# Kernel tuning notes

Hardware: AMD Instinct MI355X
Metric: run time of the kernel (lower is better)

The kernel has to match this reference:

```python
import jax, jax.numpy as jnp
import numpy as np

B, N, F, D, H, T = 32, 1024, 32, 64, 64, 4


def setup_inputs() -> dict:
    key = jax.random.key(0)
    ks = jax.random.split(key, 12)
    def w(k, shape):
        return 0.01 * jax.random.normal(k, shape, dtype=jnp.float32)
    z = lambda *s: jnp.zeros(s, jnp.float32)
    return {
        "xv": jax.random.normal(ks[0], (B, N, F), dtype=jnp.float32),
        "option": jax.random.uniform(ks[1], (B, 1), dtype=jnp.float32),
        "adj": jax.random.normal(ks[2], (N, N), dtype=jnp.float32),
        "mu1": w(ks[3], (F, D)),
        "W2": w(ks[4], (D, D)), "b2": z(D),
        "W3": w(ks[5], (D, D)), "b3": z(D),
        "W4": w(ks[6], (D, 1)), "b4": z(D),
        "Wq1": w(ks[7], (D, D)), "bq1": z(D),
        "Wq2": w(ks[8], (D, 1)), "bq2": z(D),
        "Wreg": w(ks[9], (H, 2 * D)), "breg": z(H),
        "Wq": w(ks[10], (1, H)), "bq": z(1),
    }


def reference(xv, option, adj, mu1, W2, b2, W3, b3, W4, b4,
              Wq1, bq1, Wq2, bq2, Wreg, breg, Wq, bq):
    # binary adjacency for message passing, raw weights for the mu_4 branch
    A = (adj > 0).astype(xv.dtype)                       # [N,N]
    mu_1 = jnp.maximum(xv @ mu1, 0.0)                    # [B,N,D]
    # mu_4: Linear(1,D) over every edge weight, clamp, sum over neighbors
    # (identical value every round t>=1, so computed once)
    mu4 = jnp.maximum(adj[..., None] * W4[:, 0] + b4, 0.0).sum(axis=1)[None]  # [1,N,D]
    mu3 = mu4 @ W3.T + b3                                # [1,N,D]
    mu = mu_1                                            # t = 0
    for _ in range(1, T):                                # t = 1..T-1
        mu_pool = jnp.einsum('nm,bmd->bnd', A, mu)       # neighbor aggregation
        mu2 = mu_pool @ W2.T + b2
        mu = jnp.maximum(mu_1 + mu2 + mu3, 0.0)
    mu_mean = jnp.maximum(mu.mean(axis=1, keepdims=True) @ Wq1.T + bq1, 0.0)  # [B,1,D]
    mu_aug = jnp.concatenate([mu, mu_mean], axis=1)      # [B,N+1,D]
    q2 = option.reshape(B, 1, 1) @ Wq2.T + bq2           # [B,1,D]
    q2 = jnp.broadcast_to(q2, (B, N + 1, D))
    q_ = jnp.concatenate([mu_aug, q2], axis=-1)          # [B,N+1,2D]
    qreg = jnp.maximum(q_ @ Wreg.T + breg, 0.0)          # [B,N+1,H]
    return qreg @ Wq.T + bq                              # [B,N+1,1]
```

## Files before the change

### kernel.cpp

```cpp
#include <hip/hip_runtime.h>
#include <hip/hip_bf16.h>

#define Bc 32
#define Nc 1024
#define Fc 32
#define Dc 64
#define Hc 64

typedef __bf16 bf16;
typedef __bf16 bf16x4 __attribute__((ext_vector_type(4)));
typedef __bf16 bf16x8 __attribute__((ext_vector_type(8)));
typedef float  f32x4  __attribute__((ext_vector_type(4)));

#define MS 72
#define LDS_RND_NONF 18432
#define LDS_RND_FIN  37376


__global__ void k_init(const float* __restrict__ adj, const float* __restrict__ W4,
                       const float* __restrict__ b4, const float* __restrict__ W3,
                       const float* __restrict__ b3, const float* __restrict__ b2,
                       const float* __restrict__ W2, const float* __restrict__ option,
                       const float* __restrict__ Wq2, const float* __restrict__ bq2,
                       const float* __restrict__ Wreg, const float* __restrict__ breg,
                       const float* __restrict__ xv, const float* __restrict__ mu1w,
                       bf16* __restrict__ Afrag, float* __restrict__ C3,
                       bf16* __restrict__ W2bf, float* __restrict__ c2base,
                       float* __restrict__ musum,
                       float* __restrict__ mu_1, bf16* __restrict__ Xfrag0) {
    const int id = blockIdx.x, t = threadIdx.x;
    __shared__ char smem[39424];
    if (id < 1024) {
        const int n = id;
        float* red   = (float*)smem;
        float* mu4_s = red + 256;
        const float* arow = adj + (size_t)n * Nc;
        {
            const int m0 = t * 4;
            const float4 a = *(const float4*)&arow[m0];
            bf16x4 o;
            o[0] = (bf16)((a.x > 0.f) ? 1.f : 0.f);
            o[1] = (bf16)((a.y > 0.f) ? 1.f : 0.f);
            o[2] = (bf16)((a.z > 0.f) ? 1.f : 0.f);
            o[3] = (bf16)((a.w > 0.f) ? 1.f : 0.f);
            const int g = n >> 4, lm = n & 15;
            const int k0 = m0 >> 5, q = (m0 & 31) >> 3, j = m0 & 7;
            *(bf16x4*)&Afrag[(size_t)((g * 32 + k0) * 64 + lm + 16 * q) * 8 + j] = o;
        }
        const int e = t & 63, g = t >> 6;
        const float w4e = W4[e], b4e = b4[e];
        float acc = 0.f;
        const float4* arow4 = (const float4*)(arow + g * 256);
#pragma unroll 8
        for (int j = 0; j < 64; ++j) {
            const float4 av = arow4[j];
            acc += fmaxf(fmaf(av.x, w4e, b4e), 0.f);
            acc += fmaxf(fmaf(av.y, w4e, b4e), 0.f);
            acc += fmaxf(fmaf(av.z, w4e, b4e), 0.f);
            acc += fmaxf(fmaf(av.w, w4e, b4e), 0.f);
        }
        red[t] = acc;
        __syncthreads();
        if (g == 0) mu4_s[e] = red[e] + red[64 + e] + red[128 + e] + red[192 + e];
        __syncthreads();
        if (t < 64) {
            const int d = t;
            float a = b3[d] + b2[d];
#pragma unroll
            for (int ee = 0; ee < 64; ++ee) a = fmaf(mu4_s[ee], W3[d * 64 + ee], a);
            C3[n * 64 + d] = a;
        }
    } else if (id == 1024) {
        for (int j = t * 16; j < t * 16 + 16; ++j) W2bf[j] = (bf16)W2[j];
        for (int i = t; i < 2048; i += 256) musum[i] = 0.f;
        for (int i = t; i < 2048; i += 256) {
            const int b = i >> 6, h = i & 63;
            const float opt = option[b];
            float a = breg[h];
#pragma unroll
            for (int j = 0; j < 64; ++j)
                a = fmaf(fmaf(opt, Wq2[j], bq2[j]), Wreg[h * 128 + 64 + j], a);
            c2base[i] = a;
        }
    } else {
        const int idx = id - 1025, nb = idx & 15, b = idx >> 4;
        const int n0 = nb * 64;
        const int l = t & 63, wv = t >> 6, lm = l & 15, q = l >> 4;
        bf16* W2s = (bf16*)smem;
        bf16* xhi = (bf16*)(smem + 9216);
        bf16* xlo = (bf16*)(smem + 14336);
        bf16* whi = (bf16*)(smem + 19456);
        bf16* wlo = (bf16*)(smem + 24576);
        bf16* muS = (bf16*)(smem + 29696);
        {
            const int row = t >> 2, f0 = (t & 3) * 8;
            const float* src = &xv[((size_t)b * Nc + n0 + row) * Fc + f0];
            const float4 v0 = *(const float4*)src;
            const float4 v1 = *(const float4*)(src + 4);
            bf16x8 hi, lo;
            float vv[8] = {v0.x, v0.y, v0.z, v0.w, v1.x, v1.y, v1.z, v1.w};
#pragma unroll
            for (int j = 0; j < 8; ++j) { hi[j] = (bf16)vv[j]; lo[j] = (bf16)(vv[j] - (float)hi[j]); }
            *(bf16x8*)&xhi[row * 40 + f0] = hi;
            *(bf16x8*)&xlo[row * 40 + f0] = lo;
        }
        {
            const int d = t >> 2, f0 = (t & 3) * 8;
#pragma unroll
            for (int j = 0; j < 8; ++j) {
                const float v = mu1w[(f0 + j) * Dc + d];
                const bf16 hi = (bf16)v;
                whi[d * 40 + f0 + j] = hi;
                wlo[d * 40 + f0 + j] = (bf16)(v - (float)hi);
            }
        }
        {
            const int row = t >> 2, c0 = (t & 3) * 16;
            const float4 v0 = *(const float4*)&W2[row * 64 + c0];
            const float4 v1 = *(const float4*)&W2[row * 64 + c0 + 4];
            const float4 v2 = *(const float4*)&W2[row * 64 + c0 + 8];
            const float4 v3 = *(const float4*)&W2[row * 64 + c0 + 12];
            bf16x8 p0, p1;
            p0[0]=(bf16)v0.x; p0[1]=(bf16)v0.y; p0[2]=(bf16)v0.z; p0[3]=(bf16)v0.w;
            p0[4]=(bf16)v1.x; p0[5]=(bf16)v1.y; p0[6]=(bf16)v1.z; p0[7]=(bf16)v1.w;
            p1[0]=(bf16)v2.x; p1[1]=(bf16)v2.y; p1[2]=(bf16)v2.z; p1[3]=(bf16)v2.w;
            p1[4]=(bf16)v3.x; p1[5]=(bf16)v3.y; p1[6]=(bf16)v3.z; p1[7]=(bf16)v3.w;
            *(bf16x8*)&W2s[row * MS + c0] = p0;
            *(bf16x8*)&W2s[row * MS + c0 + 8] = p1;
        }
        __syncthreads();
        f32x4 acc[4];
#pragma unroll
        for (int ct = 0; ct < 4; ++ct)
#pragma unroll
            for (int r = 0; r < 4; ++r) acc[ct][r] = 0.f;
        {
            const bf16x8 aHi = *(const bf16x8*)&xhi[(wv * 16 + lm) * 40 + q * 8];
            const bf16x8 aLo = *(const bf16x8*)&xlo[(wv * 16 + lm) * 40 + q * 8];
#pragma unroll
            for (int ct = 0; ct < 4; ++ct) {
                const bf16x8 bHi = *(const bf16x8*)&whi[(ct * 16 + lm) * 40 + q * 8];
                const bf16x8 bLo = *(const bf16x8*)&wlo[(ct * 16 + lm) * 40 + q * 8];
                acc[ct] = __builtin_amdgcn_mfma_f32_16x16x32_bf16(aHi, bHi, acc[ct], 0, 0, 0);
                acc[ct] = __builtin_amdgcn_mfma_f32_16x16x32_bf16(aLo, bHi, acc[ct], 0, 0, 0);
                acc[ct] = __builtin_amdgcn_mfma_f32_16x16x32_bf16(aHi, bLo, acc[ct], 0, 0, 0);
            }
        }
#pragma unroll
        for (int ct = 0; ct < 4; ++ct) {
            const int col = ct * 16 + lm;
#pragma unroll
            for (int r = 0; r < 4; ++r) {
                const int row = wv * 16 + q * 4 + r;
                const float v = fmaxf(acc[ct][r], 0.f);
                mu_1[((size_t)b * Nc + n0 + row) * Dc + col] = v;
                muS[row * MS + col] = (bf16)v;
            }
        }
        __syncthreads();
        f32x4 xacc[4];
#pragma unroll
        for (int ct = 0; ct < 4; ++ct)
#pragma unroll
            for (int r = 0; r < 4; ++r) xacc[ct][r] = 0.f;
#pragma unroll
        for (int s = 0; s < 2; ++s) {
            bf16x8 a = *(const bf16x8*)&muS[(wv * 16 + lm) * MS + s * 32 + q * 8];
#pragma unroll
            for (int ct = 0; ct < 4; ++ct) {
                bf16x8 bv = *(const bf16x8*)&W2s[(ct * 16 + lm) * MS + s * 32 + q * 8];
                xacc[ct] = __builtin_amdgcn_mfma_f32_16x16x32_bf16(a, bv, xacc[ct], 0, 0, 0);
            }
        }
        const int k0 = nb * 2 + (wv >> 1);
        const int q_c = (wv & 1) * 2 + (q >> 1);
        const int j0 = (q & 1) * 4;
#pragma unroll
        for (int ct = 0; ct < 4; ++ct) {
            bf16x4 p;
#pragma unroll
            for (int r = 0; r < 4; ++r) p[r] = (bf16)xacc[ct][r];
            *(bf16x4*)&Xfrag0[(size_t)b * 65536
                              + (size_t)((ct * 32 + k0) * 64 + lm + 16 * q_c) * 8 + j0] = p;
        }
    }
}

template <bool FINAL>
__global__ __launch_bounds__(256, 2)
void k_round(const bf16* __restrict__ Afrag, const bf16* __restrict__ Xfr_in,
             const float* __restrict__ mu_1, const float* __restrict__ C3,
             const bf16* __restrict__ W2bf, bf16* __restrict__ Xfr_out,
             const float* __restrict__ Wreg, const float* __restrict__ c2base,
             const float* __restrict__ Wq, const float* __restrict__ bq,
             float* __restrict__ musum, float* __restrict__ out) {
    const int id = blockIdx.x, t = threadIdx.x;
    const int b  = ((id & 7) << 2) | ((id >> 3) & 3);
    const int nb = id >> 5;
    const int n0 = nb * 64;
    const int l = t & 63, wv = t >> 6, lm = l & 15, q = l >> 4;
    const int rh = wv & 1, ch = wv >> 1;
    extern __shared__ char smem[];
    bf16* muHi = (bf16*)smem;
    bf16* muLo = (bf16*)(smem + 9216);
    bf16* WHi  = (bf16*)(smem + (FINAL ? 18432 : 9216));
    bf16* WLo  = (bf16*)(smem + 27648);
    float* rpart = (float*)(smem + 36864);

    if (!FINAL) {
#pragma unroll
        for (int i = 0; i < 2; ++i) {
            int g = i * 256 + t, row = g >> 3, c = g & 7;
            *(bf16x8*)&WHi[row * MS + c * 8] = *(const bf16x8*)&W2bf[row * 64 + c * 8];
        }
    } else {
#pragma unroll
        for (int i = 0; i < 4; ++i) {
            int g = i * 1024 + t * 4, h = g >> 6, d = g & 63;
            const float4 w4 = *(const float4*)&Wreg[h * 128 + d];
            bf16x4 ohi, olo;
            ohi[0] = (bf16)w4.x; olo[0] = (bf16)(w4.x - (float)ohi[0]);
            ohi[1] = (bf16)w4.y; olo[1] = (bf16)(w4.y - (float)ohi[1]);
            ohi[2] = (bf16)w4.z; olo[2] = (bf16)(w4.z - (float)ohi[2]);
            ohi[3] = (bf16)w4.w; olo[3] = (bf16)(w4.w - (float)ohi[3]);
            *(bf16x4*)&WHi[h * MS + d] = ohi;
            *(bf16x4*)&WLo[h * MS + d] = olo;
        }
    }

    f32x4 acc[2][2];
#pragma unroll
    for (int rt = 0; rt < 2; ++rt)
#pragma unroll
        for (int ct = 0; ct < 2; ++ct)
#pragma unroll
            for (int r = 0; r < 4; ++r) acc[rt][ct][r] = 0.f;

    const int gA = nb * 4 + rh * 2;
    const bf16* pa0 = Afrag + (size_t)(gA + 0) * 32 * 512 + l * 8;
    const bf16* pa1 = Afrag + (size_t)(gA + 1) * 32 * 512 + l * 8;
    const bf16* px0 = Xfr_in + (size_t)b * 65536 + (size_t)(ch * 2 + 0) * 32 * 512 + l * 8;
    const bf16* px1 = Xfr_in + (size_t)b * 65536 + (size_t)(ch * 2 + 1) * 32 * 512 + l * 8;
#pragma unroll 4
    for (int k0 = 0; k0 < 32; ++k0) {
        const int o = k0 * 512;
        bf16x8 a0 = *(const bf16x8*)&pa0[o];
        bf16x8 a1 = *(const bf16x8*)&pa1[o];
        bf16x8 x0 = *(const bf16x8*)&px0[o];
        bf16x8 x1 = *(const bf16x8*)&px1[o];
        acc[0][0] = __builtin_amdgcn_mfma_f32_16x16x32_bf16(a0, x0, acc[0][0], 0, 0, 0);
        acc[0][1] = __builtin_amdgcn_mfma_f32_16x16x32_bf16(a0, x1, acc[0][1], 0, 0, 0);
        acc[1][0] = __builtin_amdgcn_mfma_f32_16x16x32_bf16(a1, x0, acc[1][0], 0, 0, 0);
        acc[1][1] = __builtin_amdgcn_mfma_f32_16x16x32_bf16(a1, x1, acc[1][1], 0, 0, 0);
    }

    float vals[2][2][4];
#pragma unroll
    for (int rt = 0; rt < 2; ++rt)
#pragma unroll
        for (int ct = 0; ct < 2; ++ct) {
            const int col = ch * 32 + ct * 16 + lm;
#pragma unroll
            for (int r = 0; r < 4; ++r) {
                const int n = n0 + rh * 32 + rt * 16 + q * 4 + r;
                float v = mu_1[((size_t)b * Nc + n) * Dc + col] + acc[rt][ct][r]
                        + C3[n * 64 + col];
                vals[rt][ct][r] = fmaxf(v, 0.f);
            }
        }

#pragma unroll
    for (int rt = 0; rt < 2; ++rt)
#pragma unroll
        for (int ct = 0; ct < 2; ++ct) {
            const int col = ch * 32 + ct * 16 + lm;
#pragma unroll
            for (int r = 0; r < 4; ++r) {
                const int row = rh * 32 + rt * 16 + q * 4 + r;
                const float v = vals[rt][ct][r];
                const bf16 hi = (bf16)v;
                muHi[row * MS + col] = hi;
                if (FINAL) muLo[row * MS + col] = (bf16)(v - (float)hi);
            }
        }
    if (FINAL) {
#pragma unroll
        for (int ct = 0; ct < 2; ++ct) {
            float s = 0.f;
#pragma unroll
            for (int rt = 0; rt < 2; ++rt)
#pragma unroll
                for (int r = 0; r < 4; ++r) s += vals[rt][ct][r];
            s += __shfl_xor(s, 16);
            s += __shfl_xor(s, 32);
            if (q == 0) atomicAdd(&musum[b * 64 + ch * 32 + ct * 16 + lm], s);
        }
    }
    __syncthreads();

    f32x4 xacc[2][2];
#pragma unroll
    for (int rt = 0; rt < 2; ++rt)
#pragma unroll
        for (int ct = 0; ct < 2; ++ct)
#pragma unroll
            for (int r = 0; r < 4; ++r) xacc[rt][ct][r] = 0.f;

    if (!FINAL) {
#pragma unroll
        for (int s = 0; s < 2; ++s) {
            bf16x8 aM[2], bW[2];
#pragma unroll
            for (int rt = 0; rt < 2; ++rt)
                aM[rt] = *(const bf16x8*)&muHi[(rh * 32 + rt * 16 + lm) * MS + s * 32 + q * 8];
#pragma unroll
            for (int ct = 0; ct < 2; ++ct)
                bW[ct] = *(const bf16x8*)&WHi[(ch * 32 + ct * 16 + lm) * MS + s * 32 + q * 8];
#pragma unroll
            for (int rt = 0; rt < 2; ++rt)
#pragma unroll
                for (int ct = 0; ct < 2; ++ct)
                    xacc[rt][ct] = __builtin_amdgcn_mfma_f32_16x16x32_bf16(aM[rt], bW[ct],
                                                                           xacc[rt][ct], 0, 0, 0);
        }
        const int k0 = nb * 2 + rh;
        const int q_c0 = (q >> 1), j0 = (q & 1) * 4;
#pragma unroll
        for (int rt = 0; rt < 2; ++rt)
#pragma unroll
            for (int ct = 0; ct < 2; ++ct) {
                bf16x4 p;
#pragma unroll
                for (int r = 0; r < 4; ++r) p[r] = (bf16)xacc[rt][ct][r];
                *(bf16x4*)&Xfr_out[(size_t)b * 65536
                    + (size_t)(((ch * 2 + ct) * 32 + k0) * 64 + lm + 16 * (rt * 2 + q_c0)) * 8
                    + j0] = p;
            }
    } else {
#pragma unroll
        for (int s = 0; s < 2; ++s) {
            bf16x8 aH[2], aL[2], bH[2], bL[2];
#pragma unroll
            for (int rt = 0; rt < 2; ++rt) {
                const int ao = (rh * 32 + rt * 16 + lm) * MS + s * 32 + q * 8;
                aH[rt] = *(const bf16x8*)&muHi[ao];
                aL[rt] = *(const bf16x8*)&muLo[ao];
            }
#pragma unroll
            for (int ct = 0; ct < 2; ++ct) {
                const int bo = (ch * 32 + ct * 16 + lm) * MS + s * 32 + q * 8;
                bH[ct] = *(const bf16x8*)&WHi[bo];
                bL[ct] = *(const bf16x8*)&WLo[bo];
            }
#pragma unroll
            for (int rt = 0; rt < 2; ++rt)
#pragma unroll
                for (int ct = 0; ct < 2; ++ct) {
                    xacc[rt][ct] = __builtin_amdgcn_mfma_f32_16x16x32_bf16(aH[rt], bH[ct],
                                                                           xacc[rt][ct], 0, 0, 0);
                    xacc[rt][ct] = __builtin_amdgcn_mfma_f32_16x16x32_bf16(aL[rt], bH[ct],
                                                                           xacc[rt][ct], 0, 0, 0);
                    xacc[rt][ct] = __builtin_amdgcn_mfma_f32_16x16x32_bf16(aH[rt], bL[ct],
                                                                           xacc[rt][ct], 0, 0, 0);
                }
        }
        const float bq0 = bq[0];
        float rowsum[2][4] = {{0.f, 0.f, 0.f, 0.f}, {0.f, 0.f, 0.f, 0.f}};
#pragma unroll
        for (int ct = 0; ct < 2; ++ct) {
            const int h = ch * 32 + ct * 16 + lm;
            const float c2 = c2base[b * 64 + h];
            const float wqh = Wq[h];
#pragma unroll
            for (int rt = 0; rt < 2; ++rt)
#pragma unroll
                for (int r = 0; r < 4; ++r)
                    rowsum[rt][r] += fmaxf(xacc[rt][ct][r] + c2, 0.f) * wqh;
        }
#pragma unroll
        for (int rt = 0; rt < 2; ++rt)
#pragma unroll
            for (int r = 0; r < 4; ++r) {
                float v = rowsum[rt][r];
                v += __shfl_xor(v, 1);
                v += __shfl_xor(v, 2);
                v += __shfl_xor(v, 4);
                v += __shfl_xor(v, 8);
                if (lm == 0) rpart[ch * 64 + rh * 32 + rt * 16 + q * 4 + r] = v;
            }
        __syncthreads();
        if (t < 64)
            out[(size_t)b * (Nc + 1) + n0 + t] = rpart[t] + rpart[64 + t] + bq0;
    }
}

__global__ void k_tail(const float* __restrict__ musum, const float* __restrict__ Wq1,
                       const float* __restrict__ bq1, const float* __restrict__ Wreg,
                       const float* __restrict__ c2base, const float* __restrict__ Wq,
                       const float* __restrict__ bq, float* __restrict__ out) {
    const int b = blockIdx.x, l = threadIdx.x;
    __shared__ float mean_s[64];
    __shared__ float mp[64];
    mean_s[l] = musum[b * 64 + l] * (1.f / Nc);
    __syncthreads();
    float a = bq1[l];
#pragma unroll
    for (int e = 0; e < 64; ++e) a = fmaf(mean_s[e], Wq1[l * 64 + e], a);
    mp[l] = fmaxf(a, 0.f);
    __syncthreads();
    float h = c2base[b * 64 + l];
#pragma unroll
    for (int d = 0; d < 64; ++d) h = fmaf(mp[d], Wreg[l * 128 + d], h);
    float v = fmaxf(h, 0.f) * Wq[l];
#pragma unroll
    for (int off = 32; off; off >>= 1) v += __shfl_down(v, off);
    if (l == 0) out[(size_t)b * (Nc + 1) + Nc] = v + bq[0];
}

extern "C" void kernel_launch(void* const* d_in, const int* in_sizes, int n_in,
                              void* d_out, int out_size, void* d_ws, size_t ws_size,
                              hipStream_t stream) {
    const float* xv     = (const float*)d_in[0];
    const float* option = (const float*)d_in[1];
    const float* adj    = (const float*)d_in[2];
    const float* mu1w   = (const float*)d_in[3];
    const float* W2     = (const float*)d_in[4];
    const float* b2     = (const float*)d_in[5];
    const float* W3     = (const float*)d_in[6];
    const float* b3     = (const float*)d_in[7];
    const float* W4     = (const float*)d_in[8];
    const float* b4     = (const float*)d_in[9];
    const float* Wq1    = (const float*)d_in[10];
    const float* bq1    = (const float*)d_in[11];
    const float* Wq2    = (const float*)d_in[12];
    const float* bq2    = (const float*)d_in[13];
    const float* Wreg   = (const float*)d_in[14];
    const float* breg   = (const float*)d_in[15];
    const float* Wq     = (const float*)d_in[16];
    const float* bq     = (const float*)d_in[17];
    float* out = (float*)d_out;

    float* ws = (float*)d_ws;
    const size_t MU = (size_t)Bc * Nc * Dc;
    float* mu_1     = ws;
    float* C3       = ws + MU;
    float* c2base   = C3 + 65536;
    float* musum    = c2base + 2048;
    bf16*  Afrag    = (bf16*)(musum + 2048);
    bf16*  W2bf     = Afrag + (size_t)Nc * Nc;
    bf16*  Xf0      = W2bf + 4096;
    bf16*  Xf1      = Xf0 + MU;

    k_init<<<1537, 256, 0, stream>>>(adj, W4, b4, W3, b3, b2, W2, option, Wq2, bq2,
                                     Wreg, breg, xv, mu1w,
                                     Afrag, C3, W2bf, c2base, musum, mu_1, Xf0);
    k_round<false><<<512, 256, LDS_RND_NONF, stream>>>(
        Afrag, Xf0, mu_1, C3, W2bf, Xf1,
        nullptr, nullptr, nullptr, nullptr, nullptr, nullptr);
    k_round<false><<<512, 256, LDS_RND_NONF, stream>>>(
        Afrag, Xf1, mu_1, C3, W2bf, Xf0,
        nullptr, nullptr, nullptr, nullptr, nullptr, nullptr);
    k_round<true><<<512, 256, LDS_RND_FIN, stream>>>(
        Afrag, Xf0, mu_1, C3, nullptr, nullptr,
        Wreg, c2base, Wq, bq, musum, out);
    k_tail<<<Bc, 64, 0, stream>>>(musum, Wq1, bq1, Wreg, c2base, Wq, bq, out);
}
```

Measured before the change: 154.8 us.

## Fuse all stages into one persistent kernel with software grid barriers

Merges the init, three message-passing rounds and tail kernels into a single persistent kernel of 512 blocks. The blocks synchronise through an atomic counter barrier that is reset with a memset before launch. The init work is redistributed so each block handles two adjacency rows plus one xv tile, and W3 is staged transposed in LDS. The aim is to remove the launch gaps and tail effects between the five kernels. In exchange it depends on all 512 blocks being co-resident, and the barrier has a timeout guard that could silently break correctness.

Result: slower. 343.1 us (+121.7%).

```diff
diff --git a/kernel.cpp b/kernel.cpp
--- a/kernel.cpp
+++ b/kernel.cpp
@@ -6,6 +6,7 @@
 #define Fc 32
 #define Dc 64
 #define Hc 64
+#define NBLK 512
 
 typedef __bf16 bf16;
 typedef __bf16 bf16x4 __attribute__((ext_vector_type(4)));
@@ -13,207 +14,46 @@
 typedef float  f32x4  __attribute__((ext_vector_type(4)));
 
 #define MS 72
-#define LDS_RND_NONF 18432
-#define LDS_RND_FIN  37376
-
-
-__global__ void k_init(const float* __restrict__ adj, const float* __restrict__ W4,
-                       const float* __restrict__ b4, const float* __restrict__ W3,
-                       const float* __restrict__ b3, const float* __restrict__ b2,
-                       const float* __restrict__ W2, const float* __restrict__ option,
-                       const float* __restrict__ Wq2, const float* __restrict__ bq2,
-                       const float* __restrict__ Wreg, const float* __restrict__ breg,
-                       const float* __restrict__ xv, const float* __restrict__ mu1w,
-                       bf16* __restrict__ Afrag, float* __restrict__ C3,
-                       bf16* __restrict__ W2bf, float* __restrict__ c2base,
-                       float* __restrict__ musum,
-                       float* __restrict__ mu_1, bf16* __restrict__ Xfrag0) {
-    const int id = blockIdx.x, t = threadIdx.x;
-    __shared__ char smem[39424];
-    if (id < 1024) {
-        const int n = id;
-        float* red   = (float*)smem;
-        float* mu4_s = red + 256;
-        const float* arow = adj + (size_t)n * Nc;
-        {
-            const int m0 = t * 4;
-            const float4 a = *(const float4*)&arow[m0];
-            bf16x4 o;
-            o[0] = (bf16)((a.x > 0.f) ? 1.f : 0.f);
-            o[1] = (bf16)((a.y > 0.f) ? 1.f : 0.f);
-            o[2] = (bf16)((a.z > 0.f) ? 1.f : 0.f);
-            o[3] = (bf16)((a.w > 0.f) ? 1.f : 0.f);
-            const int g = n >> 4, lm = n & 15;
-            const int k0 = m0 >> 5, q = (m0 & 31) >> 3, j = m0 & 7;
-            *(bf16x4*)&Afrag[(size_t)((g * 32 + k0) * 64 + lm + 16 * q) * 8 + j] = o;
-        }
-        const int e = t & 63, g = t >> 6;
-        const float w4e = W4[e], b4e = b4[e];
-        float acc = 0.f;
-        const float4* arow4 = (const float4*)(arow + g * 256);
-#pragma unroll 8
-        for (int j = 0; j < 64; ++j) {
-            const float4 av = arow4[j];
-            acc += fmaxf(fmaf(av.x, w4e, b4e), 0.f);
-            acc += fmaxf(fmaf(av.y, w4e, b4e), 0.f);
-            acc += fmaxf(fmaf(av.z, w4e, b4e), 0.f);
-            acc += fmaxf(fmaf(av.w, w4e, b4e), 0.f);
-        }
-        red[t] = acc;
-        __syncthreads();
-        if (g == 0) mu4_s[e] = red[e] + red[64 + e] + red[128 + e] + red[192 + e];
-        __syncthreads();
-        if (t < 64) {
-            const int d = t;
-            float a = b3[d] + b2[d];
-#pragma unroll
-            for (int ee = 0; ee < 64; ++ee) a = fmaf(mu4_s[ee], W3[d * 64 + ee], a);
-            C3[n * 64 + d] = a;
-        }
-    } else if (id == 1024) {
-        for (int j = t * 16; j < t * 16 + 16; ++j) W2bf[j] = (bf16)W2[j];
-        for (int i = t; i < 2048; i += 256) musum[i] = 0.f;
-        for (int i = t; i < 2048; i += 256) {
-            const int b = i >> 6, h = i & 63;
-            const float opt = option[b];
-            float a = breg[h];
-#pragma unroll
-            for (int j = 0; j < 64; ++j)
-                a = fmaf(fmaf(opt, Wq2[j], bq2[j]), Wreg[h * 128 + 64 + j], a);
-            c2base[i] = a;
-        }
-    } else {
-        const int idx = id - 1025, nb = idx & 15, b = idx >> 4;
-        const int n0 = nb * 64;
-        const int l = t & 63, wv = t >> 6, lm = l & 15, q = l >> 4;
-        bf16* W2s = (bf16*)smem;
-        bf16* xhi = (bf16*)(smem + 9216);
-        bf16* xlo = (bf16*)(smem + 14336);
-        bf16* whi = (bf16*)(smem + 19456);
-        bf16* wlo = (bf16*)(smem + 24576);
-        bf16* muS = (bf16*)(smem + 29696);
-        {
-            const int row = t >> 2, f0 = (t & 3) * 8;
-            const float* src = &xv[((size_t)b * Nc + n0 + row) * Fc + f0];
-            const float4 v0 = *(const float4*)src;
-            const float4 v1 = *(const float4*)(src + 4);
-            bf16x8 hi, lo;
-            float vv[8] = {v0.x, v0.y, v0.z, v0.w, v1.x, v1.y, v1.z, v1.w};
-#pragma unroll
-            for (int j = 0; j < 8; ++j) { hi[j] = (bf16)vv[j]; lo[j] = (bf16)(vv[j] - (float)hi[j]); }
-            *(bf16x8*)&xhi[row * 40 + f0] = hi;
-            *(bf16x8*)&xlo[row * 40 + f0] = lo;
-        }
-        {
-            const int d = t >> 2, f0 = (t & 3) * 8;
-#pragma unroll
-            for (int j = 0; j < 8; ++j) {
-                const float v = mu1w[(f0 + j) * Dc + d];
-                const bf16 hi = (bf16)v;
-                whi[d * 40 + f0 + j] = hi;
-                wlo[d * 40 + f0 + j] = (bf16)(v - (float)hi);
-            }
-        }
-        {
-            const int row = t >> 2, c0 = (t & 3) * 16;
-            const float4 v0 = *(const float4*)&W2[row * 64 + c0];
-            const float4 v1 = *(const float4*)&W2[row * 64 + c0 + 4];
-            const float4 v2 = *(const float4*)&W2[row * 64 + c0 + 8];
-            const float4 v3 = *(const float4*)&W2[row * 64 + c0 + 12];
-            bf16x8 p0, p1;
-            p0[0]=(bf16)v0.x; p0[1]=(bf16)v0.y; p0[2]=(bf16)v0.z; p0[3]=(bf16)v0.w;
-            p0[4]=(bf16)v1.x; p0[5]=(bf16)v1.y; p0[6]=(bf16)v1.z; p0[7]=(bf16)v1.w;
-            p1[0]=(bf16)v2.x; p1[1]=(bf16)v2.y; p1[2]=(bf16)v2.z; p1[3]=(bf16)v2.w;
-            p1[4]=(bf16)v3.x; p1[5]=(bf16)v3.y; p1[6]=(bf16)v3.z; p1[7]=(bf16)v3.w;
-            *(bf16x8*)&W2s[row * MS + c0] = p0;
-            *(bf16x8*)&W2s[row * MS + c0 + 8] = p1;
-        }
-        __syncthreads();
-        f32x4 acc[4];
-#pragma unroll
-        for (int ct = 0; ct < 4; ++ct)
-#pragma unroll
-            for (int r = 0; r < 4; ++r) acc[ct][r] = 0.f;
-        {
-            const bf16x8 aHi = *(const bf16x8*)&xhi[(wv * 16 + lm) * 40 + q * 8];
-            const bf16x8 aLo = *(const bf16x8*)&xlo[(wv * 16 + lm) * 40 + q * 8];
-#pragma unroll
-            for (int ct = 0; ct < 4; ++ct) {
-                const bf16x8 bHi = *(const bf16x8*)&whi[(ct * 16 + lm) * 40 + q * 8];
-                const bf16x8 bLo = *(const bf16x8*)&wlo[(ct * 16 + lm) * 40 + q * 8];
-                acc[ct] = __builtin_amdgcn_mfma_f32_16x16x32_bf16(aHi, bHi, acc[ct], 0, 0, 0);
-                acc[ct] = __builtin_amdgcn_mfma_f32_16x16x32_bf16(aLo, bHi, acc[ct], 0, 0, 0);
-                acc[ct] = __builtin_amdgcn_mfma_f32_16x16x32_bf16(aHi, bLo, acc[ct], 0, 0, 0);
-            }
-        }
-#pragma unroll
-        for (int ct = 0; ct < 4; ++ct) {
-            const int col = ct * 16 + lm;
-#pragma unroll
-            for (int r = 0; r < 4; ++r) {
-                const int row = wv * 16 + q * 4 + r;
-                const float v = fmaxf(acc[ct][r], 0.f);
-                mu_1[((size_t)b * Nc + n0 + row) * Dc + col] = v;
-                muS[row * MS + col] = (bf16)v;
-            }
-        }
-        __syncthreads();
-        f32x4 xacc[4];
-#pragma unroll
-        for (int ct = 0; ct < 4; ++ct)
-#pragma unroll
-            for (int r = 0; r < 4; ++r) xacc[ct][r] = 0.f;
-#pragma unroll
-        for (int s = 0; s < 2; ++s) {
-            bf16x8 a = *(const bf16x8*)&muS[(wv * 16 + lm) * MS + s * 32 + q * 8];
-#pragma unroll
-            for (int ct = 0; ct < 4; ++ct) {
-                bf16x8 bv = *(const bf16x8*)&W2s[(ct * 16 + lm) * MS + s * 32 + q * 8];
-                xacc[ct] = __builtin_amdgcn_mfma_f32_16x16x32_bf16(a, bv, xacc[ct], 0, 0, 0);
-            }
-        }
-        const int k0 = nb * 2 + (wv >> 1);
-        const int q_c = (wv & 1) * 2 + (q >> 1);
-        const int j0 = (q & 1) * 4;
-#pragma unroll
-        for (int ct = 0; ct < 4; ++ct) {
-            bf16x4 p;
-#pragma unroll
-            for (int r = 0; r < 4; ++r) p[r] = (bf16)xacc[ct][r];
-            *(bf16x4*)&Xfrag0[(size_t)b * 65536
-                              + (size_t)((ct * 32 + k0) * 64 + lm + 16 * q_c) * 8 + j0] = p;
-        }
-    }
+#define SMEM_BYTES 39424
+
+__device__ __forceinline__ void grid_sync(unsigned* bar, unsigned phase) {
+    __syncthreads();
+    if (threadIdx.x == 0) {
+        __threadfence();
+        atomicAdd(bar, 1u);
+        const unsigned tgt = (unsigned)NBLK * phase;
+        int guard = 0;
+        while (atomicAdd(bar, 0u) < tgt) {
+            __builtin_amdgcn_s_sleep(2);
+            if (++guard > (1 << 22)) break;
+        }
+        __threadfence();
+    }
+    __syncthreads();
 }
 
 template <bool FINAL>
-__global__ __launch_bounds__(256, 2)
-void k_round(const bf16* __restrict__ Afrag, const bf16* __restrict__ Xfr_in,
-             const float* __restrict__ mu_1, const float* __restrict__ C3,
-             const bf16* __restrict__ W2bf, bf16* __restrict__ Xfr_out,
-             const float* __restrict__ Wreg, const float* __restrict__ c2base,
-             const float* __restrict__ Wq, const float* __restrict__ bq,
-             float* __restrict__ musum, float* __restrict__ out) {
-    const int id = blockIdx.x, t = threadIdx.x;
+__device__ __forceinline__ void round_body(
+    char* smem, int id,
+    const bf16* __restrict__ Afrag, const bf16* __restrict__ Xfr_in,
+    const float* __restrict__ mu_1, const float* __restrict__ C3,
+    bf16* __restrict__ Xfr_out,
+    const float* __restrict__ Wreg, const float* __restrict__ c2base,
+    const float* __restrict__ Wq, const float* __restrict__ bq,
+    float* __restrict__ musum, float* __restrict__ out) {
+    const int t = threadIdx.x;
     const int b  = ((id & 7) << 2) | ((id >> 3) & 3);
     const int nb = id >> 5;
     const int n0 = nb * 64;
     const int l = t & 63, wv = t >> 6, lm = l & 15, q = l >> 4;
     const int rh = wv & 1, ch = wv >> 1;
-    extern __shared__ char smem[];
-    bf16* muHi = (bf16*)smem;
-    bf16* muLo = (bf16*)(smem + 9216);
-    bf16* WHi  = (bf16*)(smem + (FINAL ? 18432 : 9216));
+    bf16* WHi  = (bf16*)smem;
+    bf16* muHi = (bf16*)(smem + 9216);
+    bf16* muLo = (bf16*)(smem + 18432);
     bf16* WLo  = (bf16*)(smem + 27648);
     float* rpart = (float*)(smem + 36864);
 
-    if (!FINAL) {
-#pragma unroll
-        for (int i = 0; i < 2; ++i) {
-            int g = i * 256 + t, row = g >> 3, c = g & 7;
-            *(bf16x8*)&WHi[row * MS + c * 8] = *(const bf16x8*)&W2bf[row * 64 + c * 8];
-        }
-    } else {
+    if (FINAL) {
 #pragma unroll
         for (int i = 0; i < 4; ++i) {
             int g = i * 1024 + t * 4, h = g >> 6, d = g & 63;
@@ -394,27 +234,219 @@
     }
 }
 
-__global__ void k_tail(const float* __restrict__ musum, const float* __restrict__ Wq1,
-                       const float* __restrict__ bq1, const float* __restrict__ Wreg,
-                       const float* __restrict__ c2base, const float* __restrict__ Wq,
-                       const float* __restrict__ bq, float* __restrict__ out) {
-    const int b = blockIdx.x, l = threadIdx.x;
-    __shared__ float mean_s[64];
-    __shared__ float mp[64];
-    mean_s[l] = musum[b * 64 + l] * (1.f / Nc);
-    __syncthreads();
-    float a = bq1[l];
-#pragma unroll
-    for (int e = 0; e < 64; ++e) a = fmaf(mean_s[e], Wq1[l * 64 + e], a);
-    mp[l] = fmaxf(a, 0.f);
-    __syncthreads();
-    float h = c2base[b * 64 + l];
-#pragma unroll
-    for (int d = 0; d < 64; ++d) h = fmaf(mp[d], Wreg[l * 128 + d], h);
-    float v = fmaxf(h, 0.f) * Wq[l];
-#pragma unroll
-    for (int off = 32; off; off >>= 1) v += __shfl_down(v, off);
-    if (l == 0) out[(size_t)b * (Nc + 1) + Nc] = v + bq[0];
+__global__ __launch_bounds__(256, 2) void k_fused(
+    const float* __restrict__ adj, const float* __restrict__ W4,
+    const float* __restrict__ b4, const float* __restrict__ W3,
+    const float* __restrict__ b3, const float* __restrict__ b2,
+    const float* __restrict__ W2, const float* __restrict__ option,
+    const float* __restrict__ Wq2, const float* __restrict__ bq2,
+    const float* __restrict__ Wreg, const float* __restrict__ breg,
+    const float* __restrict__ xv, const float* __restrict__ mu1w,
+    const float* __restrict__ Wq1, const float* __restrict__ bq1,
+    const float* __restrict__ Wq, const float* __restrict__ bq,
+    bf16* __restrict__ Afrag, float* __restrict__ C3,
+    float* __restrict__ c2base, float* __restrict__ musum,
+    float* __restrict__ mu_1, bf16* __restrict__ Xf0, bf16* __restrict__ Xf1,
+    float* __restrict__ out, unsigned* __restrict__ bar) {
+    const int id = blockIdx.x, t = threadIdx.x;
+    extern __shared__ char smem[];
+
+    if (id < 8) {
+        musum[id * 256 + t] = 0.f;
+    } else if (id < 16) {
+        const int i = (id - 8) * 256 + t, b = i >> 6, h = i & 63;
+        const float opt = option[b];
+        float a = breg[h];
+#pragma unroll
+        for (int j = 0; j < 64; ++j)
+            a = fmaf(fmaf(opt, Wq2[j], bq2[j]), Wreg[h * 128 + 64 + j], a);
+        c2base[i] = a;
+    }
+    {
+        float* W3sT = (float*)smem;
+        float* red  = (float*)(smem + 16640);
+        float* mu4s = (float*)(smem + 17664);
+        for (int i = t; i < 4096; i += 256) {
+            const int r = i >> 6, c = i & 63;
+            W3sT[c * 65 + r] = W3[i];
+        }
+        for (int rr = 0; rr < 2; ++rr) {
+            const int n = id * 2 + rr;
+            const float* arow = adj + (size_t)n * Nc;
+            {
+                const int m0 = t * 4;
+                const float4 a = *(const float4*)&arow[m0];
+                bf16x4 o;
+                o[0] = (bf16)((a.x > 0.f) ? 1.f : 0.f);
+                o[1] = (bf16)((a.y > 0.f) ? 1.f : 0.f);
+                o[2] = (bf16)((a.z > 0.f) ? 1.f : 0.f);
+                o[3] = (bf16)((a.w > 0.f) ? 1.f : 0.f);
+                const int g = n >> 4, lm = n & 15;
+                const int k0 = m0 >> 5, qq = (m0 & 31) >> 3, j = m0 & 7;
+                *(bf16x4*)&Afrag[(size_t)((g * 32 + k0) * 64 + lm + 16 * qq) * 8 + j] = o;
+            }
+            const int e = t & 63, g = t >> 6;
+            const float w4e = W4[e], b4e = b4[e];
+            float acc = 0.f;
+            const float4* arow4 = (const float4*)(arow + g * 256);
+#pragma unroll 8
+            for (int j = 0; j < 64; ++j) {
+                const float4 av = arow4[j];
+                acc += fmaxf(fmaf(av.x, w4e, b4e), 0.f);
+                acc += fmaxf(fmaf(av.y, w4e, b4e), 0.f);
+                acc += fmaxf(fmaf(av.z, w4e, b4e), 0.f);
+                acc += fmaxf(fmaf(av.w, w4e, b4e), 0.f);
+            }
+            red[t] = acc;
+            __syncthreads();
+            if (g == 0) mu4s[e] = red[e] + red[64 + e] + red[128 + e] + red[192 + e];
+            __syncthreads();
+            if (t < 64) {
+                float a = b3[t] + b2[t];
+#pragma unroll
+                for (int ee = 0; ee < 64; ++ee) a = fmaf(mu4s[ee], W3sT[ee * 65 + t], a);
+                C3[n * 64 + t] = a;
+            }
+            __syncthreads();
+        }
+    }
+    {
+        const int nb = id & 15, b = id >> 4;
+        const int n0 = nb * 64;
+        const int l = t & 63, wv = t >> 6, lm = l & 15, q = l >> 4;
+        bf16* W2s = (bf16*)smem;
+        bf16* xhi = (bf16*)(smem + 9216);
+        bf16* xlo = (bf16*)(smem + 14336);
+        bf16* whi = (bf16*)(smem + 19456);
+        bf16* wlo = (bf16*)(smem + 24576);
+        bf16* muS = (bf16*)(smem + 29696);
+        {
+            const int row = t >> 2, f0 = (t & 3) * 8;
+            const float* src = &xv[((size_t)b * Nc + n0 + row) * Fc + f0];
+            const float4 v0 = *(const float4*)src;
+            const float4 v1 = *(const float4*)(src + 4);
+            bf16x8 hi, lo;
+            float vv[8] = {v0.x, v0.y, v0.z, v0.w, v1.x, v1.y, v1.z, v1.w};
+#pragma unroll
+            for (int j = 0; j < 8; ++j) { hi[j] = (bf16)vv[j]; lo[j] = (bf16)(vv[j] - (float)hi[j]); }
+            *(bf16x8*)&xhi[row * 40 + f0] = hi;
+            *(bf16x8*)&xlo[row * 40 + f0] = lo;
+        }
+        {
+            const int d = t >> 2, f0 = (t & 3) * 8;
+#pragma unroll
+            for (int j = 0; j < 8; ++j) {
+                const float v = mu1w[(f0 + j) * Dc + d];
+                const bf16 hi = (bf16)v;
+                whi[d * 40 + f0 + j] = hi;
+                wlo[d * 40 + f0 + j] = (bf16)(v - (float)hi);
+            }
+        }
+        {
+            const int row = t >> 2, c0 = (t & 3) * 16;
+            const float4 v0 = *(const float4*)&W2[row * 64 + c0];
+            const float4 v1 = *(const float4*)&W2[row * 64 + c0 + 4];
+            const float4 v2 = *(const float4*)&W2[row * 64 + c0 + 8];
+            const float4 v3 = *(const float4*)&W2[row * 64 + c0 + 12];
+            bf16x8 p0, p1;
+            p0[0]=(bf16)v0.x; p0[1]=(bf16)v0.y; p0[2]=(bf16)v0.z; p0[3]=(bf16)v0.w;
+            p0[4]=(bf16)v1.x; p0[5]=(bf16)v1.y; p0[6]=(bf16)v1.z; p0[7]=(bf16)v1.w;
+            p1[0]=(bf16)v2.x; p1[1]=(bf16)v2.y; p1[2]=(bf16)v2.z; p1[3]=(bf16)v2.w;
+            p1[4]=(bf16)v3.x; p1[5]=(bf16)v3.y; p1[6]=(bf16)v3.z; p1[7]=(bf16)v3.w;
+            *(bf16x8*)&W2s[row * MS + c0] = p0;
+            *(bf16x8*)&W2s[row * MS + c0 + 8] = p1;
+        }
+        __syncthreads();
+        f32x4 acc[4];
+#pragma unroll
+        for (int ct = 0; ct < 4; ++ct)
+#pragma unroll
+            for (int r = 0; r < 4; ++r) acc[ct][r] = 0.f;
+        {
+            const bf16x8 aHi = *(const bf16x8*)&xhi[(wv * 16 + lm) * 40 + q * 8];
+            const bf16x8 aLo = *(const bf16x8*)&xlo[(wv * 16 + lm) * 40 + q * 8];
+#pragma unroll
+            for (int ct = 0; ct < 4; ++ct) {
+                const bf16x8 bHi = *(const bf16x8*)&whi[(ct * 16 + lm) * 40 + q * 8];
+                const bf16x8 bLo = *(const bf16x8*)&wlo[(ct * 16 + lm) * 40 + q * 8];
+                acc[ct] = __builtin_amdgcn_mfma_f32_16x16x32_bf16(aHi, bHi, acc[ct], 0, 0, 0);
+                acc[ct] = __builtin_amdgcn_mfma_f32_16x16x32_bf16(aLo, bHi, acc[ct], 0, 0, 0);
+                acc[ct] = __builtin_amdgcn_mfma_f32_16x16x32_bf16(aHi, bLo, acc[ct], 0, 0, 0);
+            }
+        }
+#pragma unroll
+        for (int ct = 0; ct < 4; ++ct) {
+            const int col = ct * 16 + lm;
+#pragma unroll
+            for (int r = 0; r < 4; ++r) {
+                const int row = wv * 16 + q * 4 + r;
+                const float v = fmaxf(acc[ct][r], 0.f);
+                mu_1[((size_t)b * Nc + n0 + row) * Dc + col] = v;
+                muS[row * MS + col] = (bf16)v;
+            }
+        }
+        __syncthreads();
+        f32x4 xacc[4];
+#pragma unroll
+        for (int ct = 0; ct < 4; ++ct)
+#pragma unroll
+            for (int r = 0; r < 4; ++r) xacc[ct][r] = 0.f;
+#pragma unroll
+        for (int s = 0; s < 2; ++s) {
+            bf16x8 a = *(const bf16x8*)&muS[(wv * 16 + lm) * MS + s * 32 + q * 8];
+#pragma unroll
+            for (int ct = 0; ct < 4; ++ct) {
+                bf16x8 bv = *(const bf16x8*)&W2s[(ct * 16 + lm) * MS + s * 32 + q * 8];
+                xacc[ct] = __builtin_amdgcn_mfma_f32_16x16x32_bf16(a, bv, xacc[ct], 0, 0, 0);
+            }
+        }
+        const int k0 = nb * 2 + (wv >> 1);
+        const int q_c = (wv & 1) * 2 + (q >> 1);
+        const int j0 = (q & 1) * 4;
+#pragma unroll
+        for (int ct = 0; ct < 4; ++ct) {
+            bf16x4 p;
+#pragma unroll
+            for (int r = 0; r < 4; ++r) p[r] = (bf16)xacc[ct][r];
+            *(bf16x4*)&Xf0[(size_t)b * 65536
+                           + (size_t)((ct * 32 + k0) * 64 + lm + 16 * q_c) * 8 + j0] = p;
+        }
+    }
+    grid_sync(bar, 1);
+
+    round_body<false>(smem, id, Afrag, Xf0, mu_1, C3, Xf1,
+                      nullptr, nullptr, nullptr, nullptr, nullptr, nullptr);
+    grid_sync(bar, 2);
+    round_body<false>(smem, id, Afrag, Xf1, mu_1, C3, Xf0,
+                      nullptr, nullptr, nullptr, nullptr, nullptr, nullptr);
+    grid_sync(bar, 3);
+    round_body<true>(smem, id, Afrag, Xf0, mu_1, C3, nullptr,
+                     Wreg, c2base, Wq, bq, musum, out);
+    grid_sync(bar, 4);
+
+    if (id < 32) {
+        const int b = id;
+        float* mean_s = (float*)smem;
+        float* mp     = (float*)(smem + 1024);
+        if (t < 64) mean_s[t] = musum[b * 64 + t] * (1.f / Nc);
+        __syncthreads();
+        if (t < 64) {
+            float a = bq1[t];
+#pragma unroll
+            for (int e = 0; e < 64; ++e) a = fmaf(mean_s[e], Wq1[t * 64 + e], a);
+            mp[t] = fmaxf(a, 0.f);
+        }
+        __syncthreads();
+        if (t < 64) {
+            float h = c2base[b * 64 + t];
+#pragma unroll
+            for (int d = 0; d < 64; ++d) h = fmaf(mp[d], Wreg[t * 128 + d], h);
+            float v = fmaxf(h, 0.f) * Wq[t];
+#pragma unroll
+            for (int off = 32; off; off >>= 1) v += __shfl_down(v, off);
+            if (t == 0) out[(size_t)b * (Nc + 1) + Nc] = v + bq[0];
+        }
+    }
 }
 
 extern "C" void kernel_launch(void* const* d_in, const int* in_sizes, int n_in,
@@ -446,22 +478,14 @@
     float* C3       = ws + MU;
     float* c2base   = C3 + 65536;
     float* musum    = c2base + 2048;
-    bf16*  Afrag    = (bf16*)(musum + 2048);
-    bf16*  W2bf     = Afrag + (size_t)Nc * Nc;
-    bf16*  Xf0      = W2bf + 4096;
+    unsigned* bar   = (unsigned*)(musum + 2048);
+    bf16*  Afrag    = (bf16*)(bar + 16);
+    bf16*  Xf0      = Afrag + (size_t)Nc * Nc;
     bf16*  Xf1      = Xf0 + MU;
 
-    k_init<<<1537, 256, 0, stream>>>(adj, W4, b4, W3, b3, b2, W2, option, Wq2, bq2,
-                                     Wreg, breg, xv, mu1w,
-                                     Afrag, C3, W2bf, c2base, musum, mu_1, Xf0);
-    k_round<false><<<512, 256, LDS_RND_NONF, stream>>>(
-        Afrag, Xf0, mu_1, C3, W2bf, Xf1,
-        nullptr, nullptr, nullptr, nullptr, nullptr, nullptr);
-    k_round<false><<<512, 256, LDS_RND_NONF, stream>>>(
-        Afrag, Xf1, mu_1, C3, W2bf, Xf0,
-        nullptr, nullptr, nullptr, nullptr, nullptr, nullptr);
-    k_round<true><<<512, 256, LDS_RND_FIN, stream>>>(
-        Afrag, Xf0, mu_1, C3, nullptr, nullptr,
-        Wreg, c2base, Wq, bq, musum, out);
-    k_tail<<<Bc, 64, 0, stream>>>(musum, Wq1, bq1, Wreg, c2base, Wq, bq, out);
+    hipMemsetAsync(bar, 0, 64, stream);
+    k_fused<<<NBLK, 256, SMEM_BYTES, stream>>>(
+        adj, W4, b4, W3, b3, b2, W2, option, Wq2, bq2, Wreg, breg, xv, mu1w,
+        Wq1, bq1, Wq, bq,
+        Afrag, C3, c2base, musum, mu_1, Xf0, Xf1, out, bar);
 }
```

## Fuse three message-passing rounds and tail into one persistent kernel with grid barriers

Applied to the files above, without the earlier changes.

Replaces the three per-round launches and the tail kernel with a single persistent kernel of 512 blocks that synchronises through a software grid barrier (atomic counter plus flag spin). Intermediate feature buffers are written and read with agent-scope relaxed atomics so they are visible across blocks, and W2 is staged into LDS once instead of once per round. This removes launch gaps and kernel-boundary drains. In exchange it relies on all 512 blocks being co-resident (two per CU via launch bounds), the LDS allocation grows for all rounds, and the spin loop has a timeout guard that could silently break correctness if residency fails.

After: 173.3 us. 12.0% more time.

```diff
diff --git a/kernel.cpp b/kernel.cpp
--- a/kernel.cpp
+++ b/kernel.cpp
@@ -6,6 +6,7 @@
 #define Fc 32
 #define Dc 64
 #define Hc 64
+#define NBLK 512
 
 typedef __bf16 bf16;
 typedef __bf16 bf16x4 __attribute__((ext_vector_type(4)));
@@ -13,9 +14,48 @@
 typedef float  f32x4  __attribute__((ext_vector_type(4)));
 
 #define MS 72
-#define LDS_RND_NONF 18432
-#define LDS_RND_FIN  37376
-
+#define LDS_RND 37376
+
+
+template <bool BY>
+__device__ __forceinline__ bf16x8 ld_x8(const bf16* p) {
+    if (BY) {
+        union { unsigned long long u[2]; bf16x8 v; } r;
+        r.u[0] = __hip_atomic_load((const unsigned long long*)p,
+                                   __ATOMIC_RELAXED, __HIP_MEMORY_SCOPE_AGENT);
+        r.u[1] = __hip_atomic_load((const unsigned long long*)(p + 4),
+                                   __ATOMIC_RELAXED, __HIP_MEMORY_SCOPE_AGENT);
+        return r.v;
+    } else {
+        return *(const bf16x8*)p;
+    }
+}
+
+__device__ __forceinline__ void st_x4(bf16* p, bf16x4 v) {
+    union { bf16x4 v; unsigned long long u; } r;
+    r.v = v;
+    __hip_atomic_store((unsigned long long*)p, r.u,
+                       __ATOMIC_RELAXED, __HIP_MEMORY_SCOPE_AGENT);
+}
+
+__device__ __forceinline__ void sync_lite(unsigned* cnt, unsigned* flag, unsigned phase) {
+    asm volatile("s_waitcnt vmcnt(0)" ::: "memory");
+    __syncthreads();
+    if (threadIdx.x == 0) {
+        const unsigned old =
+            __hip_atomic_fetch_add(cnt, 1u, __ATOMIC_RELAXED, __HIP_MEMORY_SCOPE_AGENT);
+        if (old == (unsigned)NBLK * phase - 1u) {
+            __hip_atomic_store(flag, phase, __ATOMIC_RELAXED, __HIP_MEMORY_SCOPE_AGENT);
+        } else {
+            int guard = 0;
+            while (__hip_atomic_load(flag, __ATOMIC_RELAXED, __HIP_MEMORY_SCOPE_AGENT) < phase) {
+                __builtin_amdgcn_s_sleep(8);
+                if (++guard > (1 << 21)) break;
+            }
+        }
+    }
+    __syncthreads();
+}
 
 __global__ void k_init(const float* __restrict__ adj, const float* __restrict__ W4,
                        const float* __restrict__ b4, const float* __restrict__ W3,
@@ -27,7 +67,8 @@
                        bf16* __restrict__ Afrag, float* __restrict__ C3,
                        bf16* __restrict__ W2bf, float* __restrict__ c2base,
                        float* __restrict__ musum,
-                       float* __restrict__ mu_1, bf16* __restrict__ Xfrag0) {
+                       float* __restrict__ mu_1, bf16* __restrict__ Xfrag0,
+                       unsigned* __restrict__ bar) {
     const int id = blockIdx.x, t = threadIdx.x;
     __shared__ char smem[39424];
     if (id < 1024) {
@@ -73,6 +114,7 @@
     } else if (id == 1024) {
         for (int j = t * 16; j < t * 16 + 16; ++j) W2bf[j] = (bf16)W2[j];
         for (int i = t; i < 2048; i += 256) musum[i] = 0.f;
+        if (t < 64) bar[t] = 0u;
         for (int i = t; i < 2048; i += 256) {
             const int b = i >> 6, h = i & 63;
             const float opt = option[b];
@@ -186,34 +228,28 @@
     }
 }
 
-template <bool FINAL>
-__global__ __launch_bounds__(256, 2)
-void k_round(const bf16* __restrict__ Afrag, const bf16* __restrict__ Xfr_in,
-             const float* __restrict__ mu_1, const float* __restrict__ C3,
-             const bf16* __restrict__ W2bf, bf16* __restrict__ Xfr_out,
-             const float* __restrict__ Wreg, const float* __restrict__ c2base,
-             const float* __restrict__ Wq, const float* __restrict__ bq,
-             float* __restrict__ musum, float* __restrict__ out) {
-    const int id = blockIdx.x, t = threadIdx.x;
+template <bool FINAL, bool XBY>
+__device__ __forceinline__ void round_body(
+    char* smem, int id,
+    const bf16* __restrict__ Afrag, const bf16* __restrict__ Xfr_in,
+    const float* __restrict__ mu_1, const float* __restrict__ C3,
+    bf16* __restrict__ Xfr_out,
+    const float* __restrict__ Wreg, const float* __restrict__ c2base,
+    const float* __restrict__ Wq, const float* __restrict__ bq,
+    float* __restrict__ musum, float* __restrict__ out) {
+    const int t = threadIdx.x;
     const int b  = ((id & 7) << 2) | ((id >> 3) & 3);
     const int nb = id >> 5;
     const int n0 = nb * 64;
     const int l = t & 63, wv = t >> 6, lm = l & 15, q = l >> 4;
     const int rh = wv & 1, ch = wv >> 1;
-    extern __shared__ char smem[];
-    bf16* muHi = (bf16*)smem;
-    bf16* muLo = (bf16*)(smem + 9216);
-    bf16* WHi  = (bf16*)(smem + (FINAL ? 18432 : 9216));
+    bf16* WHi  = (bf16*)smem;
+    bf16* muHi = (bf16*)(smem + 9216);
+    bf16* muLo = (bf16*)(smem + 18432);
     bf16* WLo  = (bf16*)(smem + 27648);
     float* rpart = (float*)(smem + 36864);
 
-    if (!FINAL) {
-#pragma unroll
-        for (int i = 0; i < 2; ++i) {
-            int g = i * 256 + t, row = g >> 3, c = g & 7;
-            *(bf16x8*)&WHi[row * MS + c * 8] = *(const bf16x8*)&W2bf[row * 64 + c * 8];
-        }
-    } else {
+    if (FINAL) {
 #pragma unroll
         for (int i = 0; i < 4; ++i) {
             int g = i * 1024 + t * 4, h = g >> 6, d = g & 63;
@@ -246,8 +282,8 @@
         const int o = k0 * 512;
         bf16x8 a0 = *(const bf16x8*)&pa0[o];
         bf16x8 a1 = *(const bf16x8*)&pa1[o];
-        bf16x8 x0 = *(const bf16x8*)&px0[o];
-        bf16x8 x1 = *(const bf16x8*)&px1[o];
+        bf16x8 x0 = ld_x8<XBY>(&px0[o]);
+        bf16x8 x1 = ld_x8<XBY>(&px1[o]);
         acc[0][0] = __builtin_amdgcn_mfma_f32_16x16x32_bf16(a0, x0, acc[0][0], 0, 0, 0);
         acc[0][1] = __builtin_amdgcn_mfma_f32_16x16x32_bf16(a0, x1, acc[0][1], 0, 0, 0);
         acc[1][0] = __builtin_amdgcn_mfma_f32_16x16x32_bf16(a1, x0, acc[1][0], 0, 0, 0);
@@ -332,9 +368,9 @@
                 bf16x4 p;
 #pragma unroll
                 for (int r = 0; r < 4; ++r) p[r] = (bf16)xacc[rt][ct][r];
-                *(bf16x4*)&Xfr_out[(size_t)b * 65536
+                st_x4(&Xfr_out[(size_t)b * 65536
                     + (size_t)(((ch * 2 + ct) * 32 + k0) * 64 + lm + 16 * (rt * 2 + q_c0)) * 8
-                    + j0] = p;
+                    + j0], p);
             }
     } else {
 #pragma unroll
@@ -394,27 +430,66 @@
     }
 }
 
-__global__ void k_tail(const float* __restrict__ musum, const float* __restrict__ Wq1,
-                       const float* __restrict__ bq1, const float* __restrict__ Wreg,
-                       const float* __restrict__ c2base, const float* __restrict__ Wq,
-                       const float* __restrict__ bq, float* __restrict__ out) {
-    const int b = blockIdx.x, l = threadIdx.x;
-    __shared__ float mean_s[64];
-    __shared__ float mp[64];
-    mean_s[l] = musum[b * 64 + l] * (1.f / Nc);
+__global__ __launch_bounds__(256, 2) void k_rounds3(
+    const bf16* __restrict__ Afrag, bf16* __restrict__ Xf0, bf16* __restrict__ Xf1,
+    const float* __restrict__ mu_1, const float* __restrict__ C3,
+    const bf16* __restrict__ W2bf,
+    const float* __restrict__ Wreg, const float* __restrict__ c2base,
+    const float* __restrict__ Wq, const float* __restrict__ bq,
+    const float* __restrict__ Wq1, const float* __restrict__ bq1,
+    float* __restrict__ musum, float* __restrict__ out,
+    unsigned* __restrict__ bar) {
+    const int id = blockIdx.x, t = threadIdx.x;
+    extern __shared__ char smem[];
+    unsigned* cnt  = bar;
+    unsigned* flag = bar + 32;
+
+    {
+        bf16* WHi = (bf16*)smem;
+#pragma unroll
+        for (int i = 0; i < 2; ++i) {
+            int g = i * 256 + t, row = g >> 3, c = g & 7;
+            *(bf16x8*)&WHi[row * MS + c * 8] = *(const bf16x8*)&W2bf[row * 64 + c * 8];
+        }
+    }
     __syncthreads();
-    float a = bq1[l];
-#pragma unroll
-    for (int e = 0; e < 64; ++e) a = fmaf(mean_s[e], Wq1[l * 64 + e], a);
-    mp[l] = fmaxf(a, 0.f);
-    __syncthreads();
-    float h = c2base[b * 64 + l];
-#pragma unroll
-    for (int d = 0; d < 64; ++d) h = fmaf(mp[d], Wreg[l * 128 + d], h);
-    float v = fmaxf(h, 0.f) * Wq[l];
-#pragma unroll
-    for (int off = 32; off; off >>= 1) v += __shfl_down(v, off);
-    if (l == 0) out[(size_t)b * (Nc + 1) + Nc] = v + bq[0];
+
+    round_body<false, false>(smem, id, Afrag, Xf0, mu_1, C3, Xf1,
+                             nullptr, nullptr, nullptr, nullptr, nullptr, nullptr);
+    sync_lite(cnt, flag, 1);
+    round_body<false, true>(smem, id, Afrag, Xf1, mu_1, C3, Xf0,
+                            nullptr, nullptr, nullptr, nullptr, nullptr, nullptr);
+    sync_lite(cnt, flag, 2);
+    round_body<true, true>(smem, id, Afrag, Xf0, mu_1, C3, nullptr,
+                           Wreg, c2base, Wq, bq, musum, out);
+    sync_lite(cnt, flag, 3);
+
+    if (id < 32) {
+        const int b = id;
+        float* mean_s = (float*)smem;
+        float* mp     = (float*)(smem + 1024);
+        if (t < 64)
+            mean_s[t] = __hip_atomic_load(&musum[b * 64 + t],
+                                          __ATOMIC_RELAXED, __HIP_MEMORY_SCOPE_AGENT)
+                        * (1.f / Nc);
+        __syncthreads();
+        if (t < 64) {
+            float a = bq1[t];
+#pragma unroll
+            for (int e = 0; e < 64; ++e) a = fmaf(mean_s[e], Wq1[t * 64 + e], a);
+            mp[t] = fmaxf(a, 0.f);
+        }
+        __syncthreads();
+        if (t < 64) {
+            float h = c2base[b * 64 + t];
+#pragma unroll
+            for (int d = 0; d < 64; ++d) h = fmaf(mp[d], Wreg[t * 128 + d], h);
+            float v = fmaxf(h, 0.f) * Wq[t];
+#pragma unroll
+            for (int off = 32; off; off >>= 1) v += __shfl_down(v, off);
+            if (t == 0) out[(size_t)b * (Nc + 1) + Nc] = v + bq[0];
+        }
+    }
 }
 
 extern "C" void kernel_launch(void* const* d_in, const int* in_sizes, int n_in,
@@ -446,22 +521,16 @@
     float* C3       = ws + MU;
     float* c2base   = C3 + 65536;
     float* musum    = c2base + 2048;
-    bf16*  Afrag    = (bf16*)(musum + 2048);
+    unsigned* bar   = (unsigned*)(musum + 2048);
+    bf16*  Afrag    = (bf16*)(bar + 64);
     bf16*  W2bf     = Afrag + (size_t)Nc * Nc;
     bf16*  Xf0      = W2bf + 4096;
     bf16*  Xf1      = Xf0 + MU;
 
     k_init<<<1537, 256, 0, stream>>>(adj, W4, b4, W3, b3, b2, W2, option, Wq2, bq2,
                                      Wreg, breg, xv, mu1w,
-                                     Afrag, C3, W2bf, c2base, musum, mu_1, Xf0);
-    k_round<false><<<512, 256, LDS_RND_NONF, stream>>>(
-        Afrag, Xf0, mu_1, C3, W2bf, Xf1,
-        nullptr, nullptr, nullptr, nullptr, nullptr, nullptr);
-    k_round<false><<<512, 256, LDS_RND_NONF, stream>>>(
-        Afrag, Xf1, mu_1, C3, W2bf, Xf0,
-        nullptr, nullptr, nullptr, nullptr, nullptr, nullptr);
-    k_round<true><<<512, 256, LDS_RND_FIN, stream>>>(
-        Afrag, Xf0, mu_1, C3, nullptr, nullptr,
-        Wreg, c2base, Wq, bq, musum, out);
-    k_tail<<<Bc, 64, 0, stream>>>(musum, Wq1, bq1, Wreg, c2base, Wq, bq, out);
-}
+                                     Afrag, C3, W2bf, c2base, musum, mu_1, Xf0, bar);
+    k_rounds3<<<NBLK, 256, LDS_RND, stream>>>(
+        Afrag, Xf0, Xf1, mu_1, C3, W2bf,
+        Wreg, c2base, Wq, bq, Wq1, bq1, musum, out, bar);
+}
```
